# Optimization experiments

Hardware: AMD Instinct MI355X
Metric: run time of the kernel (lower is better)

Reference implementation:

```python
import jax, jax.numpy as jnp
import numpy as np

B, T, IN, H, OUT = 128, 1024, 17, 512, 17


def setup_inputs() -> dict:
    key = jax.random.key(0)
    ks = jax.random.split(key, 11)
    s_in = 1.0 / np.sqrt(H)
    return {
        "x": jax.random.normal(ks[0], (B, T, IN), dtype=jnp.float32),
        "wih0": jax.random.normal(ks[1], (4 * H, IN), dtype=jnp.float32) * s_in,
        "whh0": jax.random.normal(ks[2], (4 * H, H), dtype=jnp.float32) * s_in,
        "bih0": jax.random.normal(ks[3], (4 * H,), dtype=jnp.float32) * s_in,
        "bhh0": jax.random.normal(ks[4], (4 * H,), dtype=jnp.float32) * s_in,
        "wih1": jax.random.normal(ks[5], (4 * H, H), dtype=jnp.float32) * s_in,
        "whh1": jax.random.normal(ks[6], (4 * H, H), dtype=jnp.float32) * s_in,
        "bih1": jax.random.normal(ks[7], (4 * H,), dtype=jnp.float32) * s_in,
        "bhh1": jax.random.normal(ks[8], (4 * H,), dtype=jnp.float32) * s_in,
        "lin_w": jax.random.normal(ks[9], (OUT, H), dtype=jnp.float32) * s_in,
        "lin_b": jax.random.normal(ks[10], (OUT,), dtype=jnp.float32) * s_in,
    }


def _lstm_layer(x, wih, whh, bih, bhh):
    # x: [B, T, D]; gate order i, f, g, o (torch.nn.LSTMCell convention)
    b, _, _ = x.shape
    h = whh.shape[1]
    # Precompute input projection for all timesteps: [B, T, 4H]
    proj = jnp.einsum("btd,gd->btg", x, wih) + bih

    def step(carry, p_t):
        h_t, c_t = carry
        gates = p_t + h_t @ whh.T + bhh  # [B, 4H]
        i, f, g, o = jnp.split(gates, 4, axis=1)
        i = jax.nn.sigmoid(i)
        f = jax.nn.sigmoid(f)
        o = jax.nn.sigmoid(o)
        g = jnp.tanh(g)
        c_t = f * c_t + i * g
        h_t = o * jnp.tanh(c_t)
        return (h_t, c_t), h_t

    h0 = jnp.zeros((b, h), x.dtype)
    c0 = jnp.zeros((b, h), x.dtype)
    _, ys = jax.lax.scan(step, (h0, c0), jnp.swapaxes(proj, 0, 1))  # ys: [T, B, H]
    return jnp.swapaxes(ys, 0, 1)  # [B, T, H]


def reference(x, wih0, whh0, bih0, bhh0, wih1, whh1, bih1, bhh1, lin_w, lin_b):
    y = _lstm_layer(x, wih0, whh0, bih0, bhh0)
    y = _lstm_layer(y, wih1, whh1, bih1, bhh1)
    h_last = y[:, -1, :]  # [B, H]
    return h_last @ lin_w.T + lin_b  # [B, OUT]
```

## Files before the change

kernel.cpp:

```cpp
#include <hip/hip_runtime.h>
#include <cstddef>
#include <cstdint>

typedef unsigned long long ull;
typedef unsigned short u16;
typedef unsigned int u32;
typedef __attribute__((ext_vector_type(8))) short s8v;
typedef __attribute__((ext_vector_type(4))) float f4v;

#define GROUPS 8
#define BG     16
#define JS     16
#define TPB    256
#define NT     1024
#define HDIM   512
#define INDIM  17
#define OUTDIM 17
#define BTOT   128

#define AT_LD(p)   __hip_atomic_load((p), __ATOMIC_RELAXED, __HIP_MEMORY_SCOPE_AGENT)
#define AT_ST(p,v) __hip_atomic_store((p), (v), __ATOMIC_RELAXED, __HIP_MEMORY_SCOPE_AGENT)

#define PLANE32 8192
#define WIDX(k, b) ((((k) >> 5) * 512) + ((((k) >> 3) & 3) * 128) + ((b) * 8) + ((k) & 7))
#define SLICE(wg)  (((wg) >> 1) * 512 + ((wg) & 1) * 256)

#define RA_OFF     ((size_t)0)
#define RING_BYTES ((size_t)4 * GROUPS * PLANE32 * 4)
#define RB_OFF     (RA_OFF + RING_BYTES)
#define FB32_OFF   (RB_OFF + RING_BYTES)
#define WS_NEEDED  (FB32_OFF + (size_t)BTOT * HDIM * 4)
#define RIX32(sl, gr) (((size_t)(sl) * GROUPS + (gr)) * PLANE32)

#define L_H0   0
#define L_H1   49152
#define L_EXA  65536
#define L_EXB  69632
#define L_CTL  73728
#define LDS_SZ 81920

__device__ __forceinline__ u16 f2bf(float f) {
  unsigned int u = __float_as_uint(f);
  u += 0x7FFFu + ((u >> 16) & 1u);
  return (u16)(u >> 16);
}
__device__ __forceinline__ float bf2f(u16 h) {
  return __uint_as_float(((unsigned int)h) << 16);
}
__device__ __forceinline__ float sigm(float x) { return 1.f / (1.f + __expf(-x)); }
__device__ __forceinline__ float tanh_f(float x) { return 2.f / (1.f + __expf(-2.f * x)) - 1.f; }

#define MFMA(a, b, c) __builtin_amdgcn_mfma_f32_16x16x32_bf16((a), (b), (c), 0, 0, 0)

__device__ __forceinline__ void pbar(int* c, int& nbar, int lane) {
  ++nbar;
  if (lane == 0)
    (void)__hip_atomic_fetch_add(c, 1, __ATOMIC_RELEASE, __HIP_MEMORY_SCOPE_WORKGROUP);
  while (__hip_atomic_load(c, __ATOMIC_ACQUIRE, __HIP_MEMORY_SCOPE_WORKGROUP) < 2 * nbar) {}
}

__global__ __launch_bounds__(TPB, 1) void lstm_fused(
    const float* __restrict__ x,
    const float* __restrict__ wih0, const float* __restrict__ whh0,
    const float* __restrict__ bih0, const float* __restrict__ bhh0,
    const float* __restrict__ wih1, const float* __restrict__ whh1,
    const float* __restrict__ bih1, const float* __restrict__ bhh1,
    u32* __restrict__ ringA, u32* __restrict__ ringB,
    float* __restrict__ fb32)
{
  const int bid  = blockIdx.x;
  const int gr   = bid & 7;
  const int wg   = bid >> 3;
  const int j0   = wg * JS;
  const int tid  = threadIdx.x;
  const int wave = tid >> 6;
  const int lane = tid & 63;
  const int n    = lane & 15;
  const int q    = lane >> 4;
  const int k0   = q * 8;

  __shared__ __align__(16) char smem[LDS_SZ];
  int* ctl = (int*)(smem + L_CTL);
  float* exgA = (float*)(smem + L_EXA);
  float* exgB = (float*)(smem + L_EXB);

  if (tid < 8) ctl[tid] = 0;

  {
    int b_l = tid >> 4, j_l = tid & 15, jg = j0 + j_l;
    int wo = WIDX(jg, b_l);
    AT_ST(&ringA[RIX32(0, gr) + wo], 0u);
    AT_ST(&ringB[RIX32(0, gr) + wo], 0u);
  }
  __syncthreads();

  const f4v z = {0.f, 0.f, 0.f, 0.f};
  const int p  = (wave & 1) * 64 + lane;
  const int jq = p & 15, b0 = p >> 4;
  const int jg = j0 + jq;
  const int ho0 = (jq >> 3) * 128 + b0 * 8 + (jq & 7);
  const int ho1 = (jq >> 3) * 128 + (b0 + 8) * 8 + (jq & 7);
  const int slice = SLICE(wg);
  const int half = wave & 1;
  const int sub = (lane >> 2) * 128 + (lane & 3) * 32;
  const ull TMASK = 0xFFFF0000FFFF0000ULL;

  if (wave < 2) {
    const int g0 = wave * 2;
    s8v wx_h[2], wx_l[2];
#pragma unroll
    for (int i = 0; i < 2; ++i) {
      const float* wr = wih0 + (size_t)((g0 + i) * HDIM + j0 + n) * INDIM;
#pragma unroll
      for (int j = 0; j < 8; ++j) {
        int k = k0 + j;
        float v = (k < INDIM) ? wr[k] : 0.f;
        u16 hi = f2bf(v);
        wx_h[i][j] = (short)hi;
        wx_l[i][j] = (short)f2bf(v - bf2f(hi));
      }
    }
    s8v wh_h[2][16], wh_l[2][16];
#pragma unroll
    for (int i = 0; i < 2; ++i) {
      const float* wr = whh0 + (size_t)((g0 + i) * HDIM + j0 + n) * HDIM;
#pragma unroll
      for (int kt = 0; kt < 16; ++kt)
#pragma unroll
        for (int j = 0; j < 8; ++j) {
          float v = wr[kt * 32 + k0 + j];
          u16 hi = f2bf(v);
          wh_h[i][kt][j] = (short)hi;
          wh_l[i][kt][j] = (short)f2bf(v - bf2f(hi));
        }
    }
    float bias[4];
#pragma unroll
    for (int g = 0; g < 4; ++g) bias[g] = bih0[g * HDIM + jg] + bhh0[g * HDIM + jg];
    float c0a = 0.f, c0b = 0.f;
    int nbar = 0;

    for (int s = 1; s <= NT + 1; ++s) {
      f4v xa[2] = {z, z};
      if (s <= NT) {
        const float* xr = x + ((size_t)(gr * BG + n) * NT + (s - 1)) * INDIM;
        s8v axh, axl;
#pragma unroll
        for (int j = 0; j < 8; ++j) {
          int k = k0 + j;
          float v = (k < INDIM) ? xr[k] : 0.f;
          u16 hi = f2bf(v);
          axh[j] = (short)hi;
          axl[j] = (short)f2bf(v - bf2f(hi));
        }
#pragma unroll
        for (int i = 0; i < 2; ++i) {
          xa[i] = MFMA(axh, wx_h[i], xa[i]);
          xa[i] = MFMA(axl, wx_h[i], xa[i]);
          xa[i] = MFMA(axh, wx_l[i], xa[i]);
        }
      }
      const int sl3 = (s - 1) % 3;
      {
        const ull* src = (const ull*)(ringA + RIX32((s - 1) & 3, gr)) + half * 2048;
        const ull tg = (ull)(u16)(s - 1);
        const ull pat = (tg << 16) | (tg << 48);
        for (;;) {
          ull w = AT_LD(src + sub);
          int l1t = __hip_atomic_load(&ctl[7], __ATOMIC_ACQUIRE,
                                      __HIP_MEMORY_SCOPE_WORKGROUP);
          if (__ballot((((w ^ pat) & TMASK) == 0) & (l1t >= s - 4)) == ~0ULL) break;
          __builtin_amdgcn_s_sleep(1);
        }
        ull v[32];
        for (;;) {
          ull acc = 0;
#pragma unroll
          for (int i = 0; i < 16; ++i) {
            v[2 * i]     = AT_LD(src + (i * 64 + lane) * 2);
            v[2 * i + 1] = AT_LD(src + (i * 64 + lane) * 2 + 1);
          }
#pragma unroll
          for (int i = 0; i < 32; ++i) acc |= (v[i] ^ pat) & TMASK;
          if (__ballot(acc == 0) == ~0ULL) break;
          __builtin_amdgcn_s_sleep(1);
        }
        char* dst = smem + L_H0 + sl3 * 16384 + half * 8192;
#pragma unroll
        for (int i = 0; i < 16; ++i) {
          ull a = v[2 * i], b = v[2 * i + 1];
          ull packed = (a & 0xFFFFULL) | ((a >> 16) & 0xFFFF0000ULL)
                     | ((b & 0xFFFFULL) << 32) | (((b >> 16) & 0xFFFF0000ULL) << 32);
          *(ull*)(dst + (i * 64 + lane) * 8) = packed;
        }
      }
      pbar(&ctl[0], nbar, lane);
      if (wave == 0 && lane == 0)
        __hip_atomic_store(&ctl[4 + sl3], s - 1, __ATOMIC_RELEASE,
                           __HIP_MEMORY_SCOPE_WORKGROUP);
      if (s == NT + 1) break;

      const char* sh = smem + L_H0 + sl3 * 16384;
      f4v cHH[2] = {z, z}, cHL[2] = {z, z};
#pragma unroll
      for (int kt = 0; kt < 16; ++kt) {
        s8v ah = *(const s8v*)(sh + kt * 1024 + q * 256 + n * 16);
#pragma unroll
        for (int i = 0; i < 2; ++i) {
          cHH[i] = MFMA(ah, wh_h[i][kt], cHH[i]);
          cHL[i] = MFMA(ah, wh_l[i][kt], cHL[i]);
        }
      }
#pragma unroll
      for (int i = 0; i < 2; ++i) {
        f4v e = xa[i] + cHH[i] + cHL[i];
#pragma unroll
        for (int r = 0; r < 4; ++r)
          exgA[(g0 + i) * 256 + (q * 4 + r) * 16 + n] = e[r];
      }
      pbar(&ctl[0], nbar, lane);
      const u32 otag = ((u32)(u16)s) << 16;
      u32* d = (u32*)(ringA + RIX32(s & 3, gr) + slice);
      {
        float pi = exgA[0 * 256 + b0 * 16 + jq] + bias[0];
        float pf = exgA[1 * 256 + b0 * 16 + jq] + bias[1];
        float pg = exgA[2 * 256 + b0 * 16 + jq] + bias[2];
        float po = exgA[3 * 256 + b0 * 16 + jq] + bias[3];
        float ig = sigm(pi), fg = sigm(pf), gg = tanh_f(pg), og = sigm(po);
        c0a = fg * c0a + ig * gg;
        AT_ST(d + ho0, otag | (u32)f2bf(og * tanh_f(c0a)));
      }
      {
        float pi = exgA[0 * 256 + (b0 + 8) * 16 + jq] + bias[0];
        float pf = exgA[1 * 256 + (b0 + 8) * 16 + jq] + bias[1];
        float pg = exgA[2 * 256 + (b0 + 8) * 16 + jq] + bias[2];
        float po = exgA[3 * 256 + (b0 + 8) * 16 + jq] + bias[3];
        float ig = sigm(pi), fg = sigm(pf), gg = tanh_f(pg), og = sigm(po);
        c0b = fg * c0b + ig * gg;
        AT_ST(d + ho1, otag | (u32)f2bf(og * tanh_f(c0b)));
      }
    }
  } else {
    const int g0 = (wave - 2) * 2;
    s8v w1x[2][16], w1h[2][16];
#pragma unroll
    for (int i = 0; i < 2; ++i) {
      const float* p1 = wih1 + (size_t)((g0 + i) * HDIM + j0 + n) * HDIM;
      const float* p2 = whh1 + (size_t)((g0 + i) * HDIM + j0 + n) * HDIM;
#pragma unroll
      for (int kt = 0; kt < 16; ++kt)
#pragma unroll
        for (int j = 0; j < 8; ++j) {
          w1x[i][kt][j] = (short)f2bf(p1[kt * 32 + k0 + j]);
          w1h[i][kt][j] = (short)f2bf(p2[kt * 32 + k0 + j]);
        }
    }
    float bias[4];
#pragma unroll
    for (int g = 0; g < 4; ++g) bias[g] = bih1[g * HDIM + jg] + bhh1[g * HDIM + jg];
    float c1a = 0.f, c1b = 0.f;
    int nbar = 0;

    for (int t = 1; t <= NT; ++t) {
      {
        const ull* src = (const ull*)(ringB + RIX32((t - 1) & 3, gr)) + half * 2048;
        const ull tg = (ull)(u16)(t - 1);
        const ull pat = (tg << 16) | (tg << 48);
        for (;;) {
          ull w = AT_LD(src + sub);
          if (__ballot(((w ^ pat) & TMASK) == 0) == ~0ULL) break;
          __builtin_amdgcn_s_sleep(1);
        }
        ull v[32];
        for (;;) {
          ull acc = 0;
#pragma unroll
          for (int i = 0; i < 16; ++i) {
            v[2 * i]     = AT_LD(src + (i * 64 + lane) * 2);
            v[2 * i + 1] = AT_LD(src + (i * 64 + lane) * 2 + 1);
          }
#pragma unroll
          for (int i = 0; i < 32; ++i) acc |= (v[i] ^ pat) & TMASK;
          if (__ballot(acc == 0) == ~0ULL) break;
          __builtin_amdgcn_s_sleep(1);
        }
        char* dst = smem + L_H1 + half * 8192;
#pragma unroll
        for (int i = 0; i < 16; ++i) {
          ull a = v[2 * i], b = v[2 * i + 1];
          ull packed = (a & 0xFFFFULL) | ((a >> 16) & 0xFFFF0000ULL)
                     | ((b & 0xFFFFULL) << 32) | (((b >> 16) & 0xFFFF0000ULL) << 32);
          *(ull*)(dst + (i * 64 + lane) * 8) = packed;
        }
      }
      pbar(&ctl[1], nbar, lane);
      const char* th = smem + L_H1;
      f4v dHH[2] = {z, z};
#pragma unroll
      for (int kt = 0; kt < 16; ++kt) {
        s8v ah = *(const s8v*)(th + kt * 1024 + q * 256 + n * 16);
#pragma unroll
        for (int i = 0; i < 2; ++i) dHH[i] = MFMA(ah, w1h[i][kt], dHH[i]);
      }
      const int sl3 = t % 3;
      while (__hip_atomic_load(&ctl[4 + sl3], __ATOMIC_ACQUIRE,
                               __HIP_MEMORY_SCOPE_WORKGROUP) < t) {}
      const char* sh = smem + L_H0 + sl3 * 16384;
      f4v eHH[2] = {z, z};
#pragma unroll
      for (int kt = 0; kt < 16; ++kt) {
        s8v ah = *(const s8v*)(sh + kt * 1024 + q * 256 + n * 16);
#pragma unroll
        for (int i = 0; i < 2; ++i) eHH[i] = MFMA(ah, w1x[i][kt], eHH[i]);
      }
#pragma unroll
      for (int i = 0; i < 2; ++i) {
        f4v e = dHH[i] + eHH[i];
#pragma unroll
        for (int r = 0; r < 4; ++r)
          exgB[(g0 + i) * 256 + (q * 4 + r) * 16 + n] = e[r];
      }
      pbar(&ctl[1], nbar, lane);
      const u32 otag = ((u32)(u16)t) << 16;
      u32* d = (u32*)(ringB + RIX32(t & 3, gr) + slice);
      {
        float pi = exgB[0 * 256 + b0 * 16 + jq] + bias[0];
        float pf = exgB[1 * 256 + b0 * 16 + jq] + bias[1];
        float pg = exgB[2 * 256 + b0 * 16 + jq] + bias[2];
        float po = exgB[3 * 256 + b0 * 16 + jq] + bias[3];
        float ig = sigm(pi), fg = sigm(pf), gg = tanh_f(pg), og = sigm(po);
        c1a = fg * c1a + ig * gg;
        float h = og * tanh_f(c1a);
        AT_ST(d + ho0, otag | (u32)f2bf(h));
        if (t == NT)
          AT_ST((u32*)&fb32[(size_t)(gr * BG + b0) * HDIM + jg], __float_as_uint(h));
      }
      {
        float pi = exgB[0 * 256 + (b0 + 8) * 16 + jq] + bias[0];
        float pf = exgB[1 * 256 + (b0 + 8) * 16 + jq] + bias[1];
        float pg = exgB[2 * 256 + (b0 + 8) * 16 + jq] + bias[2];
        float po = exgB[3 * 256 + (b0 + 8) * 16 + jq] + bias[3];
        float ig = sigm(pi), fg = sigm(pf), gg = tanh_f(pg), og = sigm(po);
        c1b = fg * c1b + ig * gg;
        float h = og * tanh_f(c1b);
        AT_ST(d + ho1, otag | (u32)f2bf(h));
        if (t == NT)
          AT_ST((u32*)&fb32[(size_t)(gr * BG + b0 + 8) * HDIM + jg], __float_as_uint(h));
      }
      if (wave == 2 && lane == 0)
        __hip_atomic_store(&ctl[7], t, __ATOMIC_RELEASE,
                           __HIP_MEMORY_SCOPE_WORKGROUP);
    }
  }
}

__global__ void final_linear(const float* __restrict__ fb32,
                             const float* __restrict__ lin_w,
                             const float* __restrict__ lin_b,
                             float* __restrict__ out) {
  int b = blockIdx.x, o = threadIdx.x;
  if (o < OUTDIM) {
    float acc = lin_b[o];
    const u32* hr = (const u32*)(fb32 + (size_t)b * HDIM);
    for (int j = 0; j < HDIM; ++j) {
      float h = __uint_as_float(AT_LD(hr + j));
      acc += h * lin_w[(size_t)o * HDIM + j];
    }
    out[b * OUTDIM + o] = acc;
  }
}

__global__ void sentinel_kernel(float* __restrict__ out, int nv) {
  int i = blockIdx.x * TPB + threadIdx.x;
  if (i < nv) out[i] = 1e30f;
}

extern "C" void kernel_launch(void* const* d_in, const int* in_sizes, int n_in,
                              void* d_out, int out_size, void* d_ws, size_t ws_size,
                              hipStream_t stream) {
  (void)in_sizes; (void)n_in;
  const float* x     = (const float*)d_in[0];
  const float* wih0  = (const float*)d_in[1];
  const float* whh0  = (const float*)d_in[2];
  const float* bih0  = (const float*)d_in[3];
  const float* bhh0  = (const float*)d_in[4];
  const float* wih1  = (const float*)d_in[5];
  const float* whh1  = (const float*)d_in[6];
  const float* bih1  = (const float*)d_in[7];
  const float* bhh1  = (const float*)d_in[8];
  const float* lin_w = (const float*)d_in[9];
  const float* lin_b = (const float*)d_in[10];
  float* out = (float*)d_out;
  char* ws = (char*)d_ws;

  if (ws_size < WS_NEEDED) {
    sentinel_kernel<<<(out_size + TPB - 1) / TPB, TPB, 0, stream>>>(out, out_size);
    return;
  }

  u32* ringA  = (u32*)(ws + RA_OFF);
  u32* ringB  = (u32*)(ws + RB_OFF);
  float* fb32 = (float*)(ws + FB32_OFF);

  lstm_fused<<<256, TPB, 0, stream>>>(x, wih0, whh0, bih0, bhh0,
                                      wih1, whh1, bih1, bhh1,
                                      ringA, ringB, fb32);
  final_linear<<<BTOT, 64, 0, stream>>>(fb32, lin_w, lin_b, out);
}
```

Measured before the change: 4.641 ms.

## Interleave gate rows per MFMA tile to drop LDS exchange; add sc0 fast polling

Weight rows are reordered so each MFMA output tile holds all four gates (i,f,g,o) for one hidden unit, and operands are swapped. Each lane can then apply the LSTM cell update straight from its accumulator, which removes the LDS gate-exchange buffers and one intra-workgroup barrier per timestep in both layers. Ring polling and bulk reads now use inline-asm global loads with the sc0 cache bit and no sleep, with a fallback to atomic loads after repeated misses. Layer-1 progress is tracked with two per-wave counters instead of one. The risks are coherence subtleties with the sc0 loads and more busy spinning on memory.

```diff
diff --git a/kernel.cpp b/kernel.cpp
--- a/kernel.cpp
+++ b/kernel.cpp
@@ -7,6 +7,7 @@
 typedef unsigned int u32;
 typedef __attribute__((ext_vector_type(8))) short s8v;
 typedef __attribute__((ext_vector_type(4))) float f4v;
+typedef __attribute__((ext_vector_type(4))) u32 u32x4;
 
 #define GROUPS 8
 #define BG     16
@@ -23,7 +24,6 @@
 
 #define PLANE32 8192
 #define WIDX(k, b) ((((k) >> 5) * 512) + ((((k) >> 3) & 3) * 128) + ((b) * 8) + ((k) & 7))
-#define SLICE(wg)  (((wg) >> 1) * 512 + ((wg) & 1) * 256)
 
 #define RA_OFF     ((size_t)0)
 #define RING_BYTES ((size_t)4 * GROUPS * PLANE32 * 4)
@@ -34,10 +34,8 @@
 
 #define L_H0   0
 #define L_H1   49152
-#define L_EXA  65536
-#define L_EXB  69632
-#define L_CTL  73728
-#define LDS_SZ 81920
+#define L_CTL  65536
+#define LDS_SZ 82944
 
 __device__ __forceinline__ u16 f2bf(float f) {
   unsigned int u = __float_as_uint(f);
@@ -51,6 +49,39 @@
 __device__ __forceinline__ float tanh_f(float x) { return 2.f / (1.f + __expf(-2.f * x)) - 1.f; }
 
 #define MFMA(a, b, c) __builtin_amdgcn_mfma_f32_16x16x32_bf16((a), (b), (c), 0, 0, 0)
+
+__device__ __forceinline__ ull sc0_read8(const ull* p) {
+  ull w;
+  asm volatile("global_load_dwordx2 %0, %1, off sc0\n\ts_waitcnt vmcnt(0)"
+               : "=&v"(w) : "v"(p) : "memory");
+  return w;
+}
+__device__ __forceinline__ void sc0_read16(const char* base, u32x4 r[16]) {
+  asm volatile(
+      "global_load_dwordx4 %0, %16, off sc0\n\t"
+      "global_load_dwordx4 %1, %16, off offset:1024 sc0\n\t"
+      "global_load_dwordx4 %2, %16, off offset:2048 sc0\n\t"
+      "global_load_dwordx4 %3, %16, off offset:3072 sc0\n\t"
+      "global_load_dwordx4 %4, %17, off sc0\n\t"
+      "global_load_dwordx4 %5, %17, off offset:1024 sc0\n\t"
+      "global_load_dwordx4 %6, %17, off offset:2048 sc0\n\t"
+      "global_load_dwordx4 %7, %17, off offset:3072 sc0\n\t"
+      "global_load_dwordx4 %8, %18, off sc0\n\t"
+      "global_load_dwordx4 %9, %18, off offset:1024 sc0\n\t"
+      "global_load_dwordx4 %10, %18, off offset:2048 sc0\n\t"
+      "global_load_dwordx4 %11, %18, off offset:3072 sc0\n\t"
+      "global_load_dwordx4 %12, %19, off sc0\n\t"
+      "global_load_dwordx4 %13, %19, off offset:1024 sc0\n\t"
+      "global_load_dwordx4 %14, %19, off offset:2048 sc0\n\t"
+      "global_load_dwordx4 %15, %19, off offset:3072 sc0\n\t"
+      "s_waitcnt vmcnt(0)"
+      : "=&v"(r[0]), "=&v"(r[1]), "=&v"(r[2]), "=&v"(r[3]),
+        "=&v"(r[4]), "=&v"(r[5]), "=&v"(r[6]), "=&v"(r[7]),
+        "=&v"(r[8]), "=&v"(r[9]), "=&v"(r[10]), "=&v"(r[11]),
+        "=&v"(r[12]), "=&v"(r[13]), "=&v"(r[14]), "=&v"(r[15])
+      : "v"(base), "v"(base + 4096), "v"(base + 8192), "v"(base + 12288)
+      : "memory");
+}
 
 __device__ __forceinline__ void pbar(int* c, int& nbar, int lane) {
   ++nbar;
@@ -78,86 +109,80 @@
   const int n    = lane & 15;
   const int q    = lane >> 4;
   const int k0   = q * 8;
+  const int gidx = n & 3;
+  const int jl   = n >> 2;
 
   __shared__ __align__(16) char smem[LDS_SZ];
   int* ctl = (int*)(smem + L_CTL);
-  float* exgA = (float*)(smem + L_EXA);
-  float* exgB = (float*)(smem + L_EXB);
-
-  if (tid < 8) ctl[tid] = 0;
+
+  if (tid < 16) ctl[tid] = 0;
 
   {
-    int b_l = tid >> 4, j_l = tid & 15, jg = j0 + j_l;
-    int wo = WIDX(jg, b_l);
+    int b_l = tid >> 4, j_l = tid & 15, jgw = j0 + j_l;
+    int wo = WIDX(jgw, b_l);
     AT_ST(&ringA[RIX32(0, gr) + wo], 0u);
     AT_ST(&ringB[RIX32(0, gr) + wo], 0u);
   }
   __syncthreads();
 
   const f4v z = {0.f, 0.f, 0.f, 0.f};
-  const int p  = (wave & 1) * 64 + lane;
-  const int jq = p & 15, b0 = p >> 4;
-  const int jg = j0 + jq;
-  const int ho0 = (jq >> 3) * 128 + b0 * 8 + (jq & 7);
-  const int ho1 = (jq >> 3) * 128 + (b0 + 8) * 8 + (jq & 7);
-  const int slice = SLICE(wg);
   const int half = wave & 1;
   const int sub = (lane >> 2) * 128 + (lane & 3) * 32;
   const ull TMASK = 0xFFFF0000FFFF0000ULL;
 
   if (wave < 2) {
-    const int g0 = wave * 2;
-    s8v wx_h[2], wx_l[2];
+    int jown[2];
+    float bias[2][4];
+    s8v wxh[2], wxl[2];
+    s8v whh_[2][16], whl_[2][16];
 #pragma unroll
     for (int i = 0; i < 2; ++i) {
-      const float* wr = wih0 + (size_t)((g0 + i) * HDIM + j0 + n) * INDIM;
+      const int jc = wave * 2 + i;
+      jown[i] = j0 + jc * 4 + q;
+      const float* wr = wih0 + (size_t)(gidx * HDIM + j0 + jc * 4 + jl) * INDIM;
 #pragma unroll
       for (int j = 0; j < 8; ++j) {
         int k = k0 + j;
         float v = (k < INDIM) ? wr[k] : 0.f;
         u16 hi = f2bf(v);
-        wx_h[i][j] = (short)hi;
-        wx_l[i][j] = (short)f2bf(v - bf2f(hi));
-      }
+        wxh[i][j] = (short)hi;
+        wxl[i][j] = (short)f2bf(v - bf2f(hi));
+      }
+      const float* hr = whh0 + (size_t)(gidx * HDIM + j0 + jc * 4 + jl) * HDIM;
+#pragma unroll
+      for (int kt = 0; kt < 16; ++kt)
+#pragma unroll
+        for (int j = 0; j < 8; ++j) {
+          float v = hr[kt * 32 + k0 + j];
+          u16 hi = f2bf(v);
+          whh_[i][kt][j] = (short)hi;
+          whl_[i][kt][j] = (short)f2bf(v - bf2f(hi));
+        }
+#pragma unroll
+      for (int g = 0; g < 4; ++g)
+        bias[i][g] = bih0[g * HDIM + jown[i]] + bhh0[g * HDIM + jown[i]];
     }
-    s8v wh_h[2][16], wh_l[2][16];
-#pragma unroll
-    for (int i = 0; i < 2; ++i) {
-      const float* wr = whh0 + (size_t)((g0 + i) * HDIM + j0 + n) * HDIM;
-#pragma unroll
-      for (int kt = 0; kt < 16; ++kt)
-#pragma unroll
-        for (int j = 0; j < 8; ++j) {
-          float v = wr[kt * 32 + k0 + j];
-          u16 hi = f2bf(v);
-          wh_h[i][kt][j] = (short)hi;
-          wh_l[i][kt][j] = (short)f2bf(v - bf2f(hi));
-        }
-    }
-    float bias[4];
-#pragma unroll
-    for (int g = 0; g < 4; ++g) bias[g] = bih0[g * HDIM + jg] + bhh0[g * HDIM + jg];
-    float c0a = 0.f, c0b = 0.f;
-    int nbar = 0;
+    float cc[2] = {0.f, 0.f};
+    int nbar = 0, fast = 1, miss = 0;
 
     for (int s = 1; s <= NT + 1; ++s) {
       f4v xa[2] = {z, z};
       if (s <= NT) {
         const float* xr = x + ((size_t)(gr * BG + n) * NT + (s - 1)) * INDIM;
-        s8v axh, axl;
+        s8v bxh, bxl;
 #pragma unroll
         for (int j = 0; j < 8; ++j) {
           int k = k0 + j;
           float v = (k < INDIM) ? xr[k] : 0.f;
           u16 hi = f2bf(v);
-          axh[j] = (short)hi;
-          axl[j] = (short)f2bf(v - bf2f(hi));
+          bxh[j] = (short)hi;
+          bxl[j] = (short)f2bf(v - bf2f(hi));
         }
 #pragma unroll
         for (int i = 0; i < 2; ++i) {
-          xa[i] = MFMA(axh, wx_h[i], xa[i]);
-          xa[i] = MFMA(axl, wx_h[i], xa[i]);
-          xa[i] = MFMA(axh, wx_l[i], xa[i]);
+          xa[i] = MFMA(wxh[i], bxh, xa[i]);
+          xa[i] = MFMA(wxh[i], bxl, xa[i]);
+          xa[i] = MFMA(wxl[i], bxh, xa[i]);
         }
       }
       const int sl3 = (s - 1) % 3;
@@ -165,30 +190,59 @@
         const ull* src = (const ull*)(ringA + RIX32((s - 1) & 3, gr)) + half * 2048;
         const ull tg = (ull)(u16)(s - 1);
         const ull pat = (tg << 16) | (tg << 48);
+        int it = 0;
         for (;;) {
-          ull w = AT_LD(src + sub);
-          int l1t = __hip_atomic_load(&ctl[7], __ATOMIC_ACQUIRE,
+          ull w;
+          if (fast && ((++it) & 7) != 0) w = sc0_read8(src + sub);
+          else                           w = AT_LD(src + sub);
+          int l1a = __hip_atomic_load(&ctl[7], __ATOMIC_ACQUIRE,
                                       __HIP_MEMORY_SCOPE_WORKGROUP);
+          int l1b = __hip_atomic_load(&ctl[8], __ATOMIC_ACQUIRE,
+                                      __HIP_MEMORY_SCOPE_WORKGROUP);
+          int l1t = l1a < l1b ? l1a : l1b;
           if (__ballot((((w ^ pat) & TMASK) == 0) & (l1t >= s - 4)) == ~0ULL) break;
-          __builtin_amdgcn_s_sleep(1);
-        }
-        ull v[32];
-        for (;;) {
-          ull acc = 0;
-#pragma unroll
-          for (int i = 0; i < 16; ++i) {
-            v[2 * i]     = AT_LD(src + (i * 64 + lane) * 2);
-            v[2 * i + 1] = AT_LD(src + (i * 64 + lane) * 2 + 1);
+          if (!fast) __builtin_amdgcn_s_sleep(1);
+        }
+        u32x4 r[16];
+        bool got = false;
+        if (fast) {
+#pragma unroll 1
+          for (int att = 0; att < 2 && !got; ++att) {
+            sc0_read16((const char*)src + lane * 16, r);
+            ull acc = 0;
+#pragma unroll
+            for (int i = 0; i < 16; ++i) {
+              ull a = ((ull)r[i][1] << 32) | r[i][0];
+              ull b = ((ull)r[i][3] << 32) | r[i][2];
+              acc |= (a ^ pat) & TMASK;
+              acc |= (b ^ pat) & TMASK;
+            }
+            got = (__ballot(acc == 0) == ~0ULL);
           }
-#pragma unroll
-          for (int i = 0; i < 32; ++i) acc |= (v[i] ^ pat) & TMASK;
-          if (__ballot(acc == 0) == ~0ULL) break;
-          __builtin_amdgcn_s_sleep(1);
+          miss = got ? 0 : miss + 1;
+          if (miss >= 4) fast = 0;
+        }
+        if (!got) {
+          for (;;) {
+            ull acc = 0;
+#pragma unroll
+            for (int i = 0; i < 16; ++i) {
+              ull a = AT_LD(src + (i * 64 + lane) * 2);
+              ull b = AT_LD(src + (i * 64 + lane) * 2 + 1);
+              r[i][0] = (u32)a; r[i][1] = (u32)(a >> 32);
+              r[i][2] = (u32)b; r[i][3] = (u32)(b >> 32);
+              acc |= (a ^ pat) & TMASK;
+              acc |= (b ^ pat) & TMASK;
+            }
+            if (__ballot(acc == 0) == ~0ULL) break;
+            __builtin_amdgcn_s_sleep(1);
+          }
         }
         char* dst = smem + L_H0 + sl3 * 16384 + half * 8192;
 #pragma unroll
         for (int i = 0; i < 16; ++i) {
-          ull a = v[2 * i], b = v[2 * i + 1];
+          ull a = ((ull)r[i][1] << 32) | r[i][0];
+          ull b = ((ull)r[i][3] << 32) | r[i][2];
           ull packed = (a & 0xFFFFULL) | ((a >> 16) & 0xFFFF0000ULL)
                      | ((b & 0xFFFFULL) << 32) | (((b >> 16) & 0xFFFF0000ULL) << 32);
           *(ull*)(dst + (i * 64 + lane) * 8) = packed;
@@ -204,90 +258,102 @@
       f4v cHH[2] = {z, z}, cHL[2] = {z, z};
 #pragma unroll
       for (int kt = 0; kt < 16; ++kt) {
-        s8v ah = *(const s8v*)(sh + kt * 1024 + q * 256 + n * 16);
+        s8v bh = *(const s8v*)(sh + kt * 1024 + q * 256 + n * 16);
 #pragma unroll
         for (int i = 0; i < 2; ++i) {
-          cHH[i] = MFMA(ah, wh_h[i][kt], cHH[i]);
-          cHL[i] = MFMA(ah, wh_l[i][kt], cHL[i]);
-        }
-      }
-#pragma unroll
-      for (int i = 0; i < 2; ++i) {
-        f4v e = xa[i] + cHH[i] + cHL[i];
-#pragma unroll
-        for (int r = 0; r < 4; ++r)
-          exgA[(g0 + i) * 256 + (q * 4 + r) * 16 + n] = e[r];
-      }
-      pbar(&ctl[0], nbar, lane);
+          cHH[i] = MFMA(whh_[i][kt], bh, cHH[i]);
+          cHL[i] = MFMA(whl_[i][kt], bh, cHL[i]);
+        }
+      }
       const u32 otag = ((u32)(u16)s) << 16;
-      u32* d = (u32*)(ringA + RIX32(s & 3, gr) + slice);
-      {
-        float pi = exgA[0 * 256 + b0 * 16 + jq] + bias[0];
-        float pf = exgA[1 * 256 + b0 * 16 + jq] + bias[1];
-        float pg = exgA[2 * 256 + b0 * 16 + jq] + bias[2];
-        float po = exgA[3 * 256 + b0 * 16 + jq] + bias[3];
-        float ig = sigm(pi), fg = sigm(pf), gg = tanh_f(pg), og = sigm(po);
-        c0a = fg * c0a + ig * gg;
-        AT_ST(d + ho0, otag | (u32)f2bf(og * tanh_f(c0a)));
-      }
-      {
-        float pi = exgA[0 * 256 + (b0 + 8) * 16 + jq] + bias[0];
-        float pf = exgA[1 * 256 + (b0 + 8) * 16 + jq] + bias[1];
-        float pg = exgA[2 * 256 + (b0 + 8) * 16 + jq] + bias[2];
-        float po = exgA[3 * 256 + (b0 + 8) * 16 + jq] + bias[3];
-        float ig = sigm(pi), fg = sigm(pf), gg = tanh_f(pg), og = sigm(po);
-        c0b = fg * c0b + ig * gg;
-        AT_ST(d + ho1, otag | (u32)f2bf(og * tanh_f(c0b)));
+      u32* d = ringA + RIX32(s & 3, gr);
+#pragma unroll
+      for (int ii = 1; ii >= 0; --ii) {
+        f4v e = xa[ii] + cHH[ii] + cHL[ii];
+        float pi = e[0] + bias[ii][0], pf = e[1] + bias[ii][1];
+        float pg = e[2] + bias[ii][2], po = e[3] + bias[ii][3];
+        float ig = sigm(pi), fg = sigm(pf), gv = tanh_f(pg), og = sigm(po);
+        cc[ii] = fg * cc[ii] + ig * gv;
+        AT_ST(d + WIDX(jown[ii], n), otag | (u32)f2bf(og * tanh_f(cc[ii])));
       }
     }
   } else {
-    const int g0 = (wave - 2) * 2;
-    s8v w1x[2][16], w1h[2][16];
+    int jown[2];
+    float bias[2][4];
+    s8v w1x_[2][16], w1h_[2][16];
 #pragma unroll
     for (int i = 0; i < 2; ++i) {
-      const float* p1 = wih1 + (size_t)((g0 + i) * HDIM + j0 + n) * HDIM;
-      const float* p2 = whh1 + (size_t)((g0 + i) * HDIM + j0 + n) * HDIM;
+      const int jc = (wave - 2) * 2 + i;
+      jown[i] = j0 + jc * 4 + q;
+      const float* p1 = wih1 + (size_t)(gidx * HDIM + j0 + jc * 4 + jl) * HDIM;
+      const float* p2 = whh1 + (size_t)(gidx * HDIM + j0 + jc * 4 + jl) * HDIM;
 #pragma unroll
       for (int kt = 0; kt < 16; ++kt)
 #pragma unroll
         for (int j = 0; j < 8; ++j) {
-          w1x[i][kt][j] = (short)f2bf(p1[kt * 32 + k0 + j]);
-          w1h[i][kt][j] = (short)f2bf(p2[kt * 32 + k0 + j]);
-        }
+          w1x_[i][kt][j] = (short)f2bf(p1[kt * 32 + k0 + j]);
+          w1h_[i][kt][j] = (short)f2bf(p2[kt * 32 + k0 + j]);
+        }
+#pragma unroll
+      for (int g = 0; g < 4; ++g)
+        bias[i][g] = bih1[g * HDIM + jown[i]] + bhh1[g * HDIM + jown[i]];
     }
-    float bias[4];
-#pragma unroll
-    for (int g = 0; g < 4; ++g) bias[g] = bih1[g * HDIM + jg] + bhh1[g * HDIM + jg];
-    float c1a = 0.f, c1b = 0.f;
-    int nbar = 0;
+    float c1[2] = {0.f, 0.f};
+    int nbar = 0, fast = 1, miss = 0;
 
     for (int t = 1; t <= NT; ++t) {
       {
         const ull* src = (const ull*)(ringB + RIX32((t - 1) & 3, gr)) + half * 2048;
         const ull tg = (ull)(u16)(t - 1);
         const ull pat = (tg << 16) | (tg << 48);
+        int it = 0;
         for (;;) {
-          ull w = AT_LD(src + sub);
+          ull w;
+          if (fast && ((++it) & 7) != 0) w = sc0_read8(src + sub);
+          else                           w = AT_LD(src + sub);
           if (__ballot(((w ^ pat) & TMASK) == 0) == ~0ULL) break;
-          __builtin_amdgcn_s_sleep(1);
-        }
-        ull v[32];
-        for (;;) {
-          ull acc = 0;
-#pragma unroll
-          for (int i = 0; i < 16; ++i) {
-            v[2 * i]     = AT_LD(src + (i * 64 + lane) * 2);
-            v[2 * i + 1] = AT_LD(src + (i * 64 + lane) * 2 + 1);
+          if (!fast) __builtin_amdgcn_s_sleep(1);
+        }
+        u32x4 r[16];
+        bool got = false;
+        if (fast) {
+#pragma unroll 1
+          for (int att = 0; att < 2 && !got; ++att) {
+            sc0_read16((const char*)src + lane * 16, r);
+            ull acc = 0;
+#pragma unroll
+            for (int i = 0; i < 16; ++i) {
+              ull a = ((ull)r[i][1] << 32) | r[i][0];
+              ull b = ((ull)r[i][3] << 32) | r[i][2];
+              acc |= (a ^ pat) & TMASK;
+              acc |= (b ^ pat) & TMASK;
+            }
+            got = (__ballot(acc == 0) == ~0ULL);
           }
-#pragma unroll
-          for (int i = 0; i < 32; ++i) acc |= (v[i] ^ pat) & TMASK;
-          if (__ballot(acc == 0) == ~0ULL) break;
-          __builtin_amdgcn_s_sleep(1);
+          miss = got ? 0 : miss + 1;
+          if (miss >= 4) fast = 0;
+        }
+        if (!got) {
+          for (;;) {
+            ull acc = 0;
+#pragma unroll
+            for (int i = 0; i < 16; ++i) {
+              ull a = AT_LD(src + (i * 64 + lane) * 2);
+              ull b = AT_LD(src + (i * 64 + lane) * 2 + 1);
+              r[i][0] = (u32)a; r[i][1] = (u32)(a >> 32);
+              r[i][2] = (u32)b; r[i][3] = (u32)(b >> 32);
+              acc |= (a ^ pat) & TMASK;
+              acc |= (b ^ pat) & TMASK;
+            }
+            if (__ballot(acc == 0) == ~0ULL) break;
+            __builtin_amdgcn_s_sleep(1);
+          }
         }
         char* dst = smem + L_H1 + half * 8192;
 #pragma unroll
         for (int i = 0; i < 16; ++i) {
-          ull a = v[2 * i], b = v[2 * i + 1];
+          ull a = ((ull)r[i][1] << 32) | r[i][0];
+          ull b = ((ull)r[i][3] << 32) | r[i][2];
           ull packed = (a & 0xFFFFULL) | ((a >> 16) & 0xFFFF0000ULL)
                      | ((b & 0xFFFFULL) << 32) | (((b >> 16) & 0xFFFF0000ULL) << 32);
           *(ull*)(dst + (i * 64 + lane) * 8) = packed;
@@ -298,9 +364,9 @@
       f4v dHH[2] = {z, z};
 #pragma unroll
       for (int kt = 0; kt < 16; ++kt) {
-        s8v ah = *(const s8v*)(th + kt * 1024 + q * 256 + n * 16);
-#pragma unroll
-        for (int i = 0; i < 2; ++i) dHH[i] = MFMA(ah, w1h[i][kt], dHH[i]);
+        s8v bh = *(const s8v*)(th + kt * 1024 + q * 256 + n * 16);
+#pragma unroll
+        for (int i = 0; i < 2; ++i) dHH[i] = MFMA(w1h_[i][kt], bh, dHH[i]);
       }
       const int sl3 = t % 3;
       while (__hip_atomic_load(&ctl[4 + sl3], __ATOMIC_ACQUIRE,
@@ -309,47 +375,28 @@
       f4v eHH[2] = {z, z};
 #pragma unroll
       for (int kt = 0; kt < 16; ++kt) {
-        s8v ah = *(const s8v*)(sh + kt * 1024 + q * 256 + n * 16);
-#pragma unroll
-        for (int i = 0; i < 2; ++i) eHH[i] = MFMA(ah, w1x[i][kt], eHH[i]);
-      }
-#pragma unroll
-      for (int i = 0; i < 2; ++i) {
-        f4v e = dHH[i] + eHH[i];
-#pragma unroll
-        for (int r = 0; r < 4; ++r)
-          exgB[(g0 + i) * 256 + (q * 4 + r) * 16 + n] = e[r];
-      }
-      pbar(&ctl[1], nbar, lane);
+        s8v bh = *(const s8v*)(sh + kt * 1024 + q * 256 + n * 16);
+#pragma unroll
+        for (int i = 0; i < 2; ++i) eHH[i] = MFMA(w1x_[i][kt], bh, eHH[i]);
+      }
+      if (lane == 0)
+        __hip_atomic_store(&ctl[7 + (wave & 1)], t, __ATOMIC_RELEASE,
+                           __HIP_MEMORY_SCOPE_WORKGROUP);
       const u32 otag = ((u32)(u16)t) << 16;
-      u32* d = (u32*)(ringB + RIX32(t & 3, gr) + slice);
-      {
-        float pi = exgB[0 * 256 + b0 * 16 + jq] + bias[0];
-        float pf = exgB[1 * 256 + b0 * 16 + jq] + bias[1];
-        float pg = exgB[2 * 256 + b0 * 16 + jq] + bias[2];
-        float po = exgB[3 * 256 + b0 * 16 + jq] + bias[3];
-        float ig = sigm(pi), fg = sigm(pf), gg = tanh_f(pg), og = sigm(po);
-        c1a = fg * c1a + ig * gg;
-        float h = og * tanh_f(c1a);
-        AT_ST(d + ho0, otag | (u32)f2bf(h));
+      u32* d = ringB + RIX32(t & 3, gr);
+#pragma unroll
+      for (int ii = 1; ii >= 0; --ii) {
+        f4v e = dHH[ii] + eHH[ii];
+        float pi = e[0] + bias[ii][0], pf = e[1] + bias[ii][1];
+        float pg = e[2] + bias[ii][2], po = e[3] + bias[ii][3];
+        float ig = sigm(pi), fg = sigm(pf), gv = tanh_f(pg), og = sigm(po);
+        c1[ii] = fg * c1[ii] + ig * gv;
+        float h = og * tanh_f(c1[ii]);
+        AT_ST(d + WIDX(jown[ii], n), otag | (u32)f2bf(h));
         if (t == NT)
-          AT_ST((u32*)&fb32[(size_t)(gr * BG + b0) * HDIM + jg], __float_as_uint(h));
-      }
-      {
-        float pi = exgB[0 * 256 + (b0 + 8) * 16 + jq] + bias[0];
-        float pf = exgB[1 * 256 + (b0 + 8) * 16 + jq] + bias[1];
-        float pg = exgB[2 * 256 + (b0 + 8) * 16 + jq] + bias[2];
-        float po = exgB[3 * 256 + (b0 + 8) * 16 + jq] + bias[3];
-        float ig = sigm(pi), fg = sigm(pf), gg = tanh_f(pg), og = sigm(po);
-        c1b = fg * c1b + ig * gg;
-        float h = og * tanh_f(c1b);
-        AT_ST(d + ho1, otag | (u32)f2bf(h));
-        if (t == NT)
-          AT_ST((u32*)&fb32[(size_t)(gr * BG + b0 + 8) * HDIM + jg], __float_as_uint(h));
-      }
-      if (wave == 2 && lane == 0)
-        __hip_atomic_store(&ctl[7], t, __ATOMIC_RELEASE,
-                           __HIP_MEMORY_SCOPE_WORKGROUP);
+          AT_ST((u32*)&fb32[(size_t)(gr * BG + n) * HDIM + jown[ii]],
+                __float_as_uint(h));
+      }
     }
   }
 }
```

Measured after the change: 5.696 ms. +22.7%, slower.
